# Performance work log

Hardware: AMD Instinct MI355X
Metric: run time of the kernel (lower is better)

The kernel has to match this reference:

```python
import jax, jax.numpy as jnp
import numpy as np
from jax import lax

B, L, R = 128, 256, 36
D_TXT, D_IMG, D_SOC = 768, 2048, 10
EPS = 0.05 ** 2        # geomloss blur=0.05, p=2 -> epsilon = blur^p
N_ITERS = 20           # fixed log-domain Sinkhorn iterations
GAMMA = 0.01


def _pcost(x, y):
    # x: [B,n,d], y: [B,m,d] -> C_ij = ||x_i - y_j||^2 / 2 (geomloss p=2 cost)
    xx = jnp.sum(x * x, -1)[:, :, None]
    yy = jnp.sum(y * y, -1)[:, None, :]
    xy = jnp.einsum('bnd,bmd->bnm', x, y)
    return 0.5 * (xx + yy - 2.0 * xy)


def _sinkhorn_cost(C, loga, logb, eps, n_iters):
    # Log-domain Sinkhorn; masked points carry loga/logb = -inf (zero weight).
    f = jnp.zeros(loga.shape, C.dtype)
    g = jnp.zeros(logb.shape, C.dtype)

    def body(fg, _):
        f, g = fg
        g = -eps * jax.nn.logsumexp(loga[:, :, None] + (f[:, :, None] - C) / eps, axis=1)
        f = -eps * jax.nn.logsumexp(logb[:, None, :] + (g[:, None, :] - C) / eps, axis=2)
        return (f, g), None

    (f, g), _ = lax.scan(body, (f, g), None, length=n_iters)
    a = jnp.exp(loga)  # exp(-inf) = 0 for masked entries
    b = jnp.exp(logb)
    return jnp.sum(a * f, -1) + jnp.sum(b * g, -1)  # <a,f> + <b,g>


def _forward(txt_global, txt_region, img_global, img_region, social, attn_mask,
             W_stat, b_stat, W_gt, b_gt, W_gi, b_gi, W_rt, b_rt, W_ri, b_ri,
             W_m1, b_m1, W_m2, b_m2):
    relu = jax.nn.relu
    soc = relu(social @ W_stat + b_stat)                            # [B,100]
    tg = relu(jnp.concatenate([txt_global, soc], axis=1) @ W_gt + b_gt)  # [B,200]
    ig = relu(img_global @ W_gi + b_gi)                              # [B,200]
    h = relu((tg + ig) @ W_m1 + b_m1)
    mix_pred = h @ W_m2 + b_m2                                       # [B,2]

    tr = relu(txt_region @ W_rt + b_rt)                              # [B,L,50]
    ir = relu(img_region @ W_ri + b_ri)                              # [B,R,50]

    Bn, _, _ = tr.shape
    Rn = ir.shape[1]
    mask = attn_mask > 0
    n_words = jnp.sum(attn_mask, axis=-1).astype(tr.dtype)          # [B]
    loga = jnp.where(mask, -jnp.log(n_words)[:, None], -jnp.inf)    # uniform over valid tokens
    logb = jnp.full((Bn, Rn), -jnp.log(float(Rn)), tr.dtype)        # uniform over regions

    # Debiased Sinkhorn divergence (geomloss SamplesLoss default debias=True):
    Sxy = _sinkhorn_cost(_pcost(tr, ir), loga, logb, EPS, N_ITERS)
    Sxx = _sinkhorn_cost(_pcost(tr, tr), loga, loga, EPS, N_ITERS)
    Syy = _sinkhorn_cost(_pcost(ir, ir), logb, logb, EPS, N_ITERS)
    w_dis = Sxy - 0.5 * (Sxx + Syy)                                  # [B]

    w_pred = jnp.stack([1.0 - GAMMA * w_dis, GAMMA * w_dis], axis=1)  # [B,2]
    logit = jax.nn.softmax(jnp.maximum(mix_pred, w_pred), axis=1)
    return logit


def setup_inputs() -> dict:
    key = jax.random.key(0)
    ks = jax.random.split(key, 24)
    init = lambda k, s: (jax.random.normal(k, s) * 0.02).astype(jnp.float32)
    lengths = jax.random.randint(ks[0], (B,), 16, L + 1)             # ragged lengths
    attn_mask = (jnp.arange(L)[None, :] < lengths[:, None]).astype(jnp.int32)
    return {
        'txt_global': jax.random.normal(ks[1], (B, D_TXT), jnp.float32),
        'txt_region': jax.random.normal(ks[2], (B, L, D_TXT), jnp.float32),
        'img_global': jax.random.normal(ks[3], (B, D_IMG), jnp.float32),
        'img_region': jax.random.normal(ks[4], (B, R, D_IMG), jnp.float32),
        'social': jax.random.normal(ks[5], (B, D_SOC), jnp.float32),
        'attn_mask': attn_mask,
        'W_stat': init(ks[6], (D_SOC, 100)), 'b_stat': jnp.zeros((100,), jnp.float32),
        'W_gt': init(ks[7], (868, 200)), 'b_gt': jnp.zeros((200,), jnp.float32),
        'W_gi': init(ks[8], (D_IMG, 200)), 'b_gi': jnp.zeros((200,), jnp.float32),
        'W_rt': init(ks[9], (D_TXT, 50)), 'b_rt': jnp.zeros((50,), jnp.float32),
        'W_ri': init(ks[10], (D_IMG, 50)), 'b_ri': jnp.zeros((50,), jnp.float32),
        'W_m1': init(ks[11], (200, 100)), 'b_m1': jnp.zeros((100,), jnp.float32),
        'W_m2': init(ks[12], (100, 2)), 'b_m2': jnp.zeros((2,), jnp.float32),
    }


def reference(txt_global, txt_region, img_global, img_region, social, attn_mask,
              W_stat, b_stat, W_gt, b_gt, W_gi, b_gi, W_rt, b_rt, W_ri, b_ri,
              W_m1, b_m1, W_m2, b_m2):
    return _forward(txt_global, txt_region, img_global, img_region, social, attn_mask,
                    W_stat, b_stat, W_gt, b_gt, W_gi, b_gi, W_rt, b_rt, W_ri, b_ri,
                    W_m1, b_m1, W_m2, b_m2)
```

## Files before the change

### kernel.cpp

```cpp
#include <hip/hip_runtime.h>

typedef float        f32x4 __attribute__((ext_vector_type(4)));
typedef short        s16x8 __attribute__((ext_vector_type(8)));
typedef unsigned int u32x4 __attribute__((ext_vector_type(4)));

#define EPS_LN2      0.0017328679513998632f
#define INV_EPS_LN2  577.0780163555852f
#define LOG2_36      5.169925001442312f

__device__ __forceinline__ short f2bf(float x) {
  unsigned int u; __builtin_memcpy(&u, &x, 4);
  u = (u + 0x7FFFu + ((u >> 16) & 1u)) >> 16;
  return (short)u;
}

__device__ __forceinline__ unsigned short f2h(float x) {
  return __builtin_bit_cast(unsigned short, (_Float16)x);
}
__device__ __forceinline__ float h2f(unsigned short h) {
  return (float)__builtin_bit_cast(_Float16, h);
}

#define GLOAD16(g, l) __builtin_amdgcn_global_load_lds( \
    (const __attribute__((address_space(1))) void*)(g), \
    (__attribute__((address_space(3))) void*)(l), 16, 0, 0)

__global__ __launch_bounds__(256) void k_prep(
    const float* __restrict__ W_rt, const float* __restrict__ W_ri,
    short* __restrict__ frt, short* __restrict__ fri,
    const float* __restrict__ txt, const float* __restrict__ img,
    const float* __restrict__ social,
    const float* __restrict__ W_stat, const float* __restrict__ b_stat,
    const float* __restrict__ W_gt, const float* __restrict__ W_gi,
    float* __restrict__ pre) {
  __shared__ float sA[32][128];
  int bid = blockIdx.x;
  if (bid < 88) {
    int slot = bid * 256 + threadIdx.x;
    const float* W; short* dst; int f;
    if (slot < 6144) { W = W_rt; dst = frt; f = slot; }
    else             { W = W_ri; dst = fri; f = slot - 6144; }
    int k32 = f >> 8, rem = f & 255, ct = rem >> 6, l = rem & 63;
    int col = ct * 16 + (l & 15);
    int k0  = k32 * 32 + (l >> 4) * 8;
    s16x8 p;
#pragma unroll
    for (int c = 0; c < 8; ++c) {
      float v = (col < 50) ? W[(k0 + c) * 50 + col] : 0.f;
      p[c] = f2bf(v);
    }
    *(s16x8*)(dst + (long)f * 8) = p;
    return;
  }
  int gb = bid - 88;
  int job = gb >> 4, rb = (gb >> 2) & 3, cb = gb & 3;
  int t = threadIdx.x, r0 = rb * 32;
  const float* W; int k0, klen;
  if (job < 6)       { k0 = job * 128;       klen = 128; W = W_gt; }
  else if (job == 6) { k0 = 0;               klen = 100; W = W_gt + 768 * 200; }
  else               { k0 = (job - 7) * 128; klen = 128; W = W_gi; }
  if (job == 6) {
    for (int idx = t; idx < 4096; idx += 256) {
      int r = idx >> 7, k = idx & 127;
      float v = 0.f;
      if (k < 100) {
        v = b_stat[k];
#pragma unroll
        for (int u = 0; u < 10; ++u) v += social[(r0 + r) * 10 + u] * W_stat[u * 100 + k];
        v = fmaxf(v, 0.f);
      }
      sA[r][k] = v;
    }
  } else {
    const float* A = (job < 6) ? txt : img;
    int K_A = (job < 6) ? 768 : 2048;
    for (int idx = t; idx < 4096; idx += 256) {
      int r = idx >> 7, k = idx & 127;
      sA[r][k] = A[(r0 + r) * K_A + k0 + k];
    }
  }
  __syncthreads();
  int c = cb * 64 + (t & 63), rg = t >> 6;
  if (c < 200) {
    float acc[8];
#pragma unroll
    for (int i = 0; i < 8; ++i) acc[i] = 0.f;
    for (int k4 = 0; k4 < klen; k4 += 4) {
      float w0 = W[(k0 + k4    ) * 200 + c];
      float w1 = W[(k0 + k4 + 1) * 200 + c];
      float w2 = W[(k0 + k4 + 2) * 200 + c];
      float w3 = W[(k0 + k4 + 3) * 200 + c];
#pragma unroll
      for (int i = 0; i < 8; ++i) {
        f32x4 a = *(const f32x4*)&sA[rg * 8 + i][k4];
        acc[i] += a[0]*w0 + a[1]*w1 + a[2]*w2 + a[3]*w3;
      }
    }
    float* dst = pre + (long)job * 25600;
#pragma unroll
    for (int i = 0; i < 8; ++i)
      dst[(r0 + rg * 8 + i) * 200 + c] = acc[i];
  }
}

template<int K32>
__device__ __forceinline__ void proj_body(const float* __restrict__ A,
                                          const short* __restrict__ Bf,
                                          const float* __restrict__ bias,
                                          float* __restrict__ out, int bid,
                                          char* smem) {
  constexpr int KH = K32 / 2;
  int wave = threadIdx.x >> 6, lane = threadIdx.x & 63;
  int rg = wave >> 1, ks = wave & 1;
  int rl = lane & 15, q = lane >> 4, r7 = rl & 7;
  int row0 = bid * 32 + rg * 16;
  const int K = K32 * 32;
  char* wbuf = smem + wave * 12288;

  int ra = lane >> 3, pa = lane & 7;
  int fsw = (pa ^ ra) * 4;
  const float* asrc0 = A + (long)(row0 + ra)     * K + ks * (KH * 32) + fsw;
  const float* asrc1 = A + (long)(row0 + 8 + ra) * K + ks * (KH * 32) + fsw;
  const short* bsrc  = Bf + (long)ks * (KH * 2048) + lane * 8;

#define PSTAGE(KK, ST) { \
    char* ad = wbuf + (ST) * 6144; \
    GLOAD16(asrc0 + (KK) * 32, ad); \
    GLOAD16(asrc1 + (KK) * 32, ad + 1024); \
    char* bd = ad + 2048; \
    const short* bs = bsrc + (KK) * 2048; \
    GLOAD16(bs,        bd); \
    GLOAD16(bs + 512,  bd + 1024); \
    GLOAD16(bs + 1024, bd + 2048); \
    GLOAD16(bs + 1536, bd + 3072); \
  }

  f32x4 acc[4];
#pragma unroll
  for (int ct = 0; ct < 4; ++ct) acc[ct] = (f32x4){0.f, 0.f, 0.f, 0.f};

  PSTAGE(0, 0);
#pragma unroll
  for (int k = 0; k < KH; ++k) {
    if (k + 1 < KH) {
      PSTAGE(k + 1, (k + 1) & 1);
      asm volatile("s_waitcnt vmcnt(6)" ::: "memory");
    } else {
      asm volatile("s_waitcnt vmcnt(0)" ::: "memory");
    }
    __builtin_amdgcn_sched_barrier(0);
    const char* ab = wbuf + (k & 1) * 6144;
    f32x4 a0 = *(const f32x4*)(ab + rl * 128 + (((q * 2)     ^ r7) << 4));
    f32x4 a1 = *(const f32x4*)(ab + rl * 128 + (((q * 2 + 1) ^ r7) << 4));
    const char* bb = ab + 2048;
    s16x8 af;
    af[0]=f2bf(a0[0]); af[1]=f2bf(a0[1]); af[2]=f2bf(a0[2]); af[3]=f2bf(a0[3]);
    af[4]=f2bf(a1[0]); af[5]=f2bf(a1[1]); af[6]=f2bf(a1[2]); af[7]=f2bf(a1[3]);
#pragma unroll
    for (int ct = 0; ct < 4; ++ct) {
      s16x8 bfr = *(const s16x8*)(bb + ct * 1024 + lane * 16);
      acc[ct] = __builtin_amdgcn_mfma_f32_16x16x32_bf16(af, bfr, acc[ct], 0, 0, 0);
    }
  }
#undef PSTAGE

  if (ks == 1) {
#pragma unroll
    for (int ct = 0; ct < 4; ++ct)
      *(f32x4*)(wbuf + ct * 1024 + lane * 16) = acc[ct];
  }
  __syncthreads();
  if (ks == 0) {
    const char* pb = smem + (wave + 1) * 12288;
#pragma unroll
    for (int ct = 0; ct < 4; ++ct) {
      f32x4 o = *(const f32x4*)(pb + ct * 1024 + lane * 16);
      int col = ct * 16 + rl;
      float bv = (col < 50) ? bias[col] : 0.f;
#pragma unroll
      for (int r = 0; r < 4; ++r) {
        int grow = row0 + q * 4 + r;
        float v = fmaxf(acc[ct][r] + o[r] + bv, 0.f);
        out[(long)grow * 64 + col] = (col < 50) ? v : 0.f;
      }
    }
  }
}

__device__ __forceinline__ void mix_body(
    int r, const float* __restrict__ pre,
    const float* __restrict__ b_gt, const float* __restrict__ b_gi,
    const float* __restrict__ W_m1, const float* __restrict__ b_m1,
    const float* __restrict__ W_m2, const float* __restrict__ b_m2,
    float* __restrict__ mix, float* smem) {
  float* sm = smem;
  float* sh = smem + 200;
  int t = threadIdx.x;
  if (t < 200) {
    float s1 = b_gt[t], s2 = b_gi[t];
#pragma unroll
    for (int j = 0; j < 7; ++j)  s1 += pre[(long)j * 25600 + r * 200 + t];
#pragma unroll
    for (int j = 7; j < 23; ++j) s2 += pre[(long)j * 25600 + r * 200 + t];
    sm[t] = fmaxf(s1, 0.f) + fmaxf(s2, 0.f);
  }
  __syncthreads();
  if (t < 100) {
    float a = b_m1[t];
#pragma unroll 4
    for (int k = 0; k < 200; ++k) a += sm[k] * W_m1[k * 100 + t];
    sh[t] = fmaxf(a, 0.f);
  }
  __syncthreads();
  if (t < 2) {
    float a = b_m2[t];
    for (int k = 0; k < 100; ++k) a += sh[k] * W_m2[k * 2 + t];
    mix[r * 2 + t] = a;
  }
}

__global__ __launch_bounds__(256)
void k_pm(
    const float* __restrict__ txt_region, const short* __restrict__ frt,
    const float* __restrict__ b_rt, float* __restrict__ tr,
    const float* __restrict__ img_region, const short* __restrict__ fri,
    const float* __restrict__ b_ri, float* __restrict__ ir,
    const float* __restrict__ pre,
    const float* __restrict__ b_gt, const float* __restrict__ b_gi,
    const float* __restrict__ W_m1, const float* __restrict__ b_m1,
    const float* __restrict__ W_m2, const float* __restrict__ b_m2,
    float* __restrict__ mix) {
  __shared__ __align__(16) char smem[49152];
  int bid = blockIdx.x;
  if (bid < 144)       proj_body<64>(img_region, fri, b_ri, ir, bid, smem);
  else if (bid < 1168) proj_body<24>(txt_region, frt, b_rt, tr, bid - 144, smem);
  else                 mix_body(bid - 1168, pre, b_gt, b_gi, W_m1, b_m1, W_m2, b_m2, mix, (float*)smem);
}

#define SK_SMEM 139264

__global__ __launch_bounds__(1024)
void k_sink(
    const float* __restrict__ tr, const float* __restrict__ ir,
    const int* __restrict__ amask,
    float* __restrict__ Sxy, float* __restrict__ Sxx, float* __restrict__ Syy) {
  __shared__ __align__(16) char smem[SK_SMEM];
  int role = blockIdx.x >> 7;
  int b    = blockIdx.x & 127;
  int tid  = threadIdx.x;

  if (role == 0) {
    short*     Xf    = (short*)smem;
    char*      CT    = smem;
    float*     norms = (float*)(smem + 131072);
    float*     sPm   = (float*)(smem + 132096);
    float*     sF    = (float*)(smem + 136192);
    float*     sG    = (float*)(smem + 137216);
    _Float16*  sAh   = (_Float16*)(smem + 138240);
    int*       nsh   = (int*)  (smem + 138784);
    if (tid < 64) {
      int c = 0;
      for (int i = tid; i < 256; i += 64) c += amask[b * 256 + i];
#pragma unroll
      for (int o = 1; o < 64; o <<= 1) c += __shfl_xor(c, o);
      if (tid == 0) *nsh = c;
    }
    const float* Xg = tr + (long)b * 256 * 64;
    for (int slot = tid; slot < 2048; slot += 1024) {
      int t = slot >> 7, k32 = (slot >> 6) & 1, l = slot & 63;
      int row = t * 16 + (l & 15), k0 = k32 * 32 + (l >> 4) * 8;
      const float* src = Xg + row * 64 + k0;
      f32x4 a0 = *(const f32x4*)src, a1 = *(const f32x4*)(src + 4);
      s16x8 p;
      p[0]=f2bf(a0[0]); p[1]=f2bf(a0[1]); p[2]=f2bf(a0[2]); p[3]=f2bf(a0[3]);
      p[4]=f2bf(a1[0]); p[5]=f2bf(a1[1]); p[6]=f2bf(a1[2]); p[7]=f2bf(a1[3]);
      *(s16x8*)(Xf + slot * 8) = p;
    }
    __syncthreads();
    int n = *nsh;
    int wv = tid >> 6, lane = tid & 63, q = lane >> 4;
    f32x4 acc[16];
#pragma unroll
    for (int ct = 0; ct < 16; ++ct) acc[ct] = (f32x4){0.f, 0.f, 0.f, 0.f};
    s16x8 afr0 = *(const s16x8*)(Xf + ((wv * 2 + 0) * 64 + lane) * 8);
    s16x8 afr1 = *(const s16x8*)(Xf + ((wv * 2 + 1) * 64 + lane) * 8);
#pragma unroll
    for (int ct = 0; ct < 16; ++ct) {
      s16x8 b0 = *(const s16x8*)(Xf + ((ct * 2 + 0) * 64 + lane) * 8);
      s16x8 b1 = *(const s16x8*)(Xf + ((ct * 2 + 1) * 64 + lane) * 8);
      acc[ct] = __builtin_amdgcn_mfma_f32_16x16x32_bf16(afr0, b0, acc[ct], 0, 0, 0);
      acc[ct] = __builtin_amdgcn_mfma_f32_16x16x32_bf16(afr1, b1, acc[ct], 0, 0, 0);
    }
#pragma unroll
    for (int r = 0; r < 4; ++r) {
      int m_ = q * 4 + r;
      if ((lane & 15) == m_) norms[wv * 16 + m_] = acc[wv][r];
    }
    __syncthreads();
    int i0w = wv * 16 + q * 4;
    float ni0 = norms[i0w], ni1 = norms[i0w + 1];
    float ni2 = norms[i0w + 2], ni3 = norms[i0w + 3];
#pragma unroll
    for (int ct = 0; ct < 16; ++ct) {
      int j = ct * 16 + (lane & 15);
      float nj = norms[j];
      float v0 = (acc[ct][0] - 0.5f * (ni0 + nj)) * INV_EPS_LN2;
      float v1 = (acc[ct][1] - 0.5f * (ni1 + nj)) * INV_EPS_LN2;
      float v2 = (acc[ct][2] - 0.5f * (ni2 + nj)) * INV_EPS_LN2;
      float v3 = (acc[ct][3] - 0.5f * (ni3 + nj)) * INV_EPS_LN2;
      char* p = CT + (((j << 9) + (i0w << 1)) ^ ((j & 7) << 4));
      unsigned p01 = (unsigned)f2h(v0) | ((unsigned)f2h(v1) << 16);
      unsigned p23 = (unsigned)f2h(v2) | ((unsigned)f2h(v3) << 16);
      *(unsigned*)(p)     = p01;
      *(unsigned*)(p + 4) = p23;
    }
    float log2n = log2f((float)n);
    if (tid < 256) {
      sF[tid] = 0.f;
      sAh[tid] = (tid < n) ? (_Float16)(-log2n) : (_Float16)(-65504.f);
    }
    __syncthreads();
    int kk = tid >> 8, j = tid & 255, i0 = kk * 64;
    unsigned base = (unsigned)((j << 9) + (i0 << 1));
    unsigned sw   = (unsigned)((j & 7) << 4);
    const unsigned* ah2 = (const unsigned*)(sAh) + kk * 32;
    for (int h = 0; h < 40; ++h) {
      unsigned mm = 0xFBFFFBFFu;
#pragma unroll
      for (int s = 0; s < 8; ++s) {
        u32x4 v = *(const u32x4*)(CT + ((base + (s << 4)) ^ sw));
        unsigned a0 = ah2[s * 4 + 0], a1 = ah2[s * 4 + 1];
        unsigned a2 = ah2[s * 4 + 2], a3 = ah2[s * 4 + 3];
        unsigned t0, t1, t2, t3;
        asm("v_pk_add_f16 %0, %1, %2" : "=v"(t0) : "v"(v[0]), "v"(a0));
        asm("v_pk_add_f16 %0, %1, %2" : "=v"(t1) : "v"(v[1]), "v"(a1));
        asm("v_pk_add_f16 %0, %1, %2" : "=v"(t2) : "v"(v[2]), "v"(a2));
        asm("v_pk_add_f16 %0, %1, %2" : "=v"(t3) : "v"(v[3]), "v"(a3));
        asm("v_pk_max_f16 %0, %0, %1" : "+v"(mm) : "v"(t0));
        asm("v_pk_max_f16 %0, %0, %1" : "+v"(mm) : "v"(t1));
        asm("v_pk_max_f16 %0, %0, %1" : "+v"(mm) : "v"(t2));
        asm("v_pk_max_f16 %0, %0, %1" : "+v"(mm) : "v"(t3));
      }
      sPm[kk * 256 + j] = fmaxf(h2f((unsigned short)(mm & 0xFFFFu)),
                                h2f((unsigned short)(mm >> 16)));
      __syncthreads();
      if (tid < 256) {
        float m4 = fmaxf(fmaxf(sPm[tid], sPm[256 + tid]),
                         fmaxf(sPm[512 + tid], sPm[768 + tid]));
        if (tid < n) {
          ((h & 1) ? sF : sG)[tid] = -EPS_LN2 * m4;
          sAh[tid] = (_Float16)(-log2n - m4);
        }
      }
      __syncthreads();
    }
    if (tid < 64) {
      float a = 0.f;
      for (int i = tid; i < n; i += 64) a += sF[i] + sG[i];
#pragma unroll
      for (int o = 1; o < 64; o <<= 1) a += __shfl_xor(a, o);
      if (tid == 0) Sxx[b] = a / n;
    }
  } else if (role == 1) {
    float* Ys  = (float*)smem;
    float* Cs  = (float*)(smem + 9216);
    float* nx  = (float*)(smem + 47104);
    float* ny  = (float*)(smem + 48128);
    float* sA  = (float*)(smem + 48288);
    float* sB  = (float*)(smem + 49376);
    float* sF  = (float*)(smem + 49536);
    float* sG  = (float*)(smem + 50560);
    int*   nsh = (int*)  (smem + 50720);
    if (tid < 64) {
      int c = 0;
      for (int i = tid; i < 256; i += 64) c += amask[b * 256 + i];
#pragma unroll
      for (int o = 1; o < 64; o <<= 1) c += __shfl_xor(c, o);
      if (tid == 0) *nsh = c;
    }
    const float* Xg = tr + (long)b * 256 * 64;
    const float* Yg = ir + (long)b * 36 * 64;
    for (int idx = tid; idx < 576; idx += 1024) {
      int row = idx >> 4, q4 = idx & 15;
      *(f32x4*)(Ys + row * 64 + q4 * 4) = *(const f32x4*)(Yg + row * 64 + q4 * 4);
    }
    __syncthreads();
    int n = *nsh;
    if (tid < 256) {
      float a = 0.f;
#pragma unroll
      for (int q4 = 0; q4 < 13; ++q4) {
        f32x4 v = *(const f32x4*)(Xg + tid * 64 + q4 * 4);
        a += v[0]*v[0] + v[1]*v[1] + v[2]*v[2] + v[3]*v[3];
      }
      nx[tid] = a;
    } else if (tid < 292) {
      int jj = tid - 256; float a = 0.f;
#pragma unroll
      for (int q4 = 0; q4 < 13; ++q4) {
        f32x4 v = *(const f32x4*)(Ys + jj * 64 + q4 * 4);
        a += v[0]*v[0] + v[1]*v[1] + v[2]*v[2] + v[3]*v[3];
      }
      ny[jj] = a;
    }
    __syncthreads();
    if (tid < 1008) {
      int ii = tid / 36, jj = tid - ii * 36;
      f32x4 yr[13];
#pragma unroll
      for (int q4 = 0; q4 < 13; ++q4) yr[q4] = *(const f32x4*)(Ys + jj * 64 + q4 * 4);
      float nyj = ny[jj];
      for (int i = ii; i < 256; i += 28) {
        float d = 0.f;
#pragma unroll
        for (int q4 = 0; q4 < 13; ++q4) {
          f32x4 xv = *(const f32x4*)(Xg + i * 64 + q4 * 4);
          d += xv[0]*yr[q4][0] + xv[1]*yr[q4][1] + xv[2]*yr[q4][2] + xv[3]*yr[q4][3];
        }
        Cs[i * 37 + jj] = (d - 0.5f * (nx[i] + nyj)) * INV_EPS_LN2;
      }
    }
    __syncthreads();
    int jg = tid >> 4, kg = tid & 15;
    float Cg[16];
    if (jg < 36) {
#pragma unroll
      for (int t = 0; t < 16; ++t) Cg[t] = Cs[(kg * 16 + t) * 37 + jg];
    }
    int fi = tid >> 2, kf = tid & 3;
    float Cf[9];
#pragma unroll
    for (int t = 0; t < 9; ++t) {
      int jj2 = kf * 9 + t;
      Cf[t] = (jj2 < 36) ? Cs[fi * 37 + jj2] : 0.f;
    }
    float log2n = log2f((float)n);
    if (tid < 256) { sF[tid] = 0.f; sA[tid + (tid >> 4)] = -log2n; }
    __syncthreads();
    const float* agp = sA + kg * 17;
    int gend = n - kg * 16; if (gend > 16) gend = 16;
    for (int it = 0; it < 20; ++it) {
      float gm = -1e30f;
      if (jg < 36) {
#pragma unroll
        for (int t = 0; t < 16; ++t)
          if (t < gend) gm = fmaxf(gm, agp[t] + Cg[t]);
        gm = fmaxf(gm, __shfl_xor(gm, 1)); gm = fmaxf(gm, __shfl_xor(gm, 2));
        gm = fmaxf(gm, __shfl_xor(gm, 4)); gm = fmaxf(gm, __shfl_xor(gm, 8));
      }
      __syncthreads();
      if (jg < 36 && kg == 0) {
        sG[jg] = -EPS_LN2 * gm;
        sB[jg] = -LOG2_36 - gm;
      }
      __syncthreads();
      float fm = -1e30f;
#pragma unroll
      for (int t = 0; t < 9; ++t) {
        int jj2 = kf * 9 + t;
        if (jj2 < 36) fm = fmaxf(fm, sB[jj2] + Cf[t]);
      }
      fm = fmaxf(fm, __shfl_xor(fm, 1)); fm = fmaxf(fm, __shfl_xor(fm, 2));
      __syncthreads();
      if (kf == 0 && fi < n) {
        sF[fi] = -EPS_LN2 * fm;
        sA[fi + (fi >> 4)] = -log2n - fm;
      }
      __syncthreads();
    }
    if (tid < 64) {
      float a = 0.f;
      for (int i = tid; i < n; i += 64) a += sF[i];
      float g = (tid < 36) ? sG[tid] : 0.f;
#pragma unroll
      for (int o = 1; o < 64; o <<= 1) { a += __shfl_xor(a, o); g += __shfl_xor(g, o); }
      if (tid == 0) Sxy[b] = a / n + g / 36.f;
    }
  } else {
    float* Ys = (float*)smem;
    float* Cs = (float*)(smem + 9216);
    float* ny = (float*)(smem + 48128);
    float* sA = (float*)(smem + 48288);
    float* sF = (float*)(smem + 49536);
    float* sG = (float*)(smem + 50560);
    const float* Yg = ir + (long)b * 36 * 64;
    for (int idx = tid; idx < 576; idx += 1024) {
      int row = idx >> 4, q4 = idx & 15;
      *(f32x4*)(Ys + row * 64 + q4 * 4) = *(const f32x4*)(Yg + row * 64 + q4 * 4);
    }
    __syncthreads();
    if (tid < 36) {
      float a = 0.f;
#pragma unroll
      for (int q4 = 0; q4 < 13; ++q4) {
        f32x4 v = *(const f32x4*)(Ys + tid * 64 + q4 * 4);
        a += v[0]*v[0] + v[1]*v[1] + v[2]*v[2] + v[3]*v[3];
      }
      ny[tid] = a;
    }
    __syncthreads();
    if (tid < 1008) {
      int ii = tid / 36, jj = tid - ii * 36;
      f32x4 yr[13];
#pragma unroll
      for (int q4 = 0; q4 < 13; ++q4) yr[q4] = *(const f32x4*)(Ys + jj * 64 + q4 * 4);
      float nyj = ny[jj];
      for (int i = ii; i < 36; i += 28) {
        float d = 0.f;
#pragma unroll
        for (int q4 = 0; q4 < 13; ++q4) {
          f32x4 xv = *(const f32x4*)(Ys + i * 64 + q4 * 4);
          d += xv[0]*yr[q4][0] + xv[1]*yr[q4][1] + xv[2]*yr[q4][2] + xv[3]*yr[q4][3];
        }
        Cs[i * 37 + jj] = (d - 0.5f * (ny[i] + nyj)) * INV_EPS_LN2;
      }
    }
    __syncthreads();
    int j = tid >> 2, kk = tid & 3;
    float Creg[9];
    if (j < 36) {
#pragma unroll
      for (int t = 0; t < 9; ++t) {
        int i2 = kk * 9 + t;
        Creg[t] = (i2 < 36) ? Cs[i2 * 37 + j] : 0.f;
      }
    }
    if (tid < 36) { sF[tid] = 0.f; sA[tid] = -LOG2_36; }
    __syncthreads();
    for (int h = 0; h < 40; ++h) {
      float m = -1e30f;
      if (j < 36) {
#pragma unroll
        for (int t = 0; t < 9; ++t) {
          int i2 = kk * 9 + t;
          if (i2 < 36) m = fmaxf(m, sA[i2] + Creg[t]);
        }
        m = fmaxf(m, __shfl_xor(m, 1)); m = fmaxf(m, __shfl_xor(m, 2));
      }
      __syncthreads();
      if (j < 36 && kk == 0) {
        ((h & 1) ? sF : sG)[j] = -EPS_LN2 * m;
        sA[j] = -LOG2_36 - m;
      }
      __syncthreads();
    }
    if (tid < 64) {
      float a = (tid < 36) ? sF[tid] + sG[tid] : 0.f;
#pragma unroll
      for (int o = 1; o < 64; o <<= 1) a += __shfl_xor(a, o);
      if (tid == 0) Syy[b] = a / 36.f;
    }
  }
}

__global__ void k_final(const float* __restrict__ mix, const float* __restrict__ sxy,
                        const float* __restrict__ sxx, const float* __restrict__ syy,
                        float* __restrict__ out) {
  int b = blockIdx.x * 64 + threadIdx.x;
  if (b < 128) {
    float w  = sxy[b] - 0.5f * (sxx[b] + syy[b]);
    float x0 = fmaxf(mix[b * 2 + 0], 1.0f - 0.01f * w);
    float x1 = fmaxf(mix[b * 2 + 1], 0.01f * w);
    float mx = fmaxf(x0, x1);
    float e0 = expf(x0 - mx), e1 = expf(x1 - mx);
    float inv = 1.f / (e0 + e1);
    out[b * 2 + 0] = e0 * inv;
    out[b * 2 + 1] = e1 * inv;
  }
}

extern "C" void kernel_launch(void* const* d_in, const int* in_sizes, int n_in,
                              void* d_out, int out_size, void* d_ws, size_t ws_size,
                              hipStream_t stream) {
  const float* txt_global = (const float*)d_in[0];
  const float* txt_region = (const float*)d_in[1];
  const float* img_global = (const float*)d_in[2];
  const float* img_region = (const float*)d_in[3];
  const float* social     = (const float*)d_in[4];
  const int*   attn_mask  = (const int*)  d_in[5];
  const float* W_stat = (const float*)d_in[6];  const float* b_stat = (const float*)d_in[7];
  const float* W_gt   = (const float*)d_in[8];  const float* b_gt   = (const float*)d_in[9];
  const float* W_gi   = (const float*)d_in[10]; const float* b_gi   = (const float*)d_in[11];
  const float* W_rt   = (const float*)d_in[12]; const float* b_rt   = (const float*)d_in[13];
  const float* W_ri   = (const float*)d_in[14]; const float* b_ri   = (const float*)d_in[15];
  const float* W_m1   = (const float*)d_in[16]; const float* b_m1   = (const float*)d_in[17];
  const float* W_m2   = (const float*)d_in[18]; const float* b_m2   = (const float*)d_in[19];

  float* ws = (float*)d_ws;
  float* ws_mix = ws;
  float* ws_sxy = ws + 256;
  float* ws_sxx = ws + 384;
  float* ws_syy = ws + 512;
  short* ws_frt = (short*)(ws + 1024);
  short* ws_fri = (short*)(ws + 25600);
  float* ws_tr  = ws + 131072;
  float* ws_ir  = ws + 2228224;
  float* ws_pre = ws + 2523136;

  k_prep<<<456, 256, 0, stream>>>(W_rt, W_ri, ws_frt, ws_fri,
                                  txt_global, img_global, social,
                                  W_stat, b_stat, W_gt, W_gi, ws_pre);
  k_pm<<<1296, 256, 0, stream>>>(txt_region, ws_frt, b_rt, ws_tr,
                                 img_region, ws_fri, b_ri, ws_ir,
                                 ws_pre, b_gt, b_gi,
                                 W_m1, b_m1, W_m2, b_m2, ws_mix);
  k_sink<<<384, 1024, 0, stream>>>(ws_tr, ws_ir, attn_mask,
                                   ws_sxy, ws_sxx, ws_syy);
  k_final<<<2, 64, 0, stream>>>(ws_mix, ws_sxy, ws_sxx, ws_syy, (float*)d_out);
}
```

Baseline: 326.4 us.

## Split Sxx Sinkhorn into separate 256-thread kernel and triple-buffer projection loads

Moves the text-text self Sinkhorn out of the fused 1024-thread kernel into its own 256-thread kernel. Each thread owns one column and scans only the valid rows, with ping-pong f16 potential buffers, so the per-iteration partial-max exchange and one barrier go away. The projection GEMM changes from double to triple buffering of its global-to-LDS loads, with deeper vmcnt waits. The costs are fewer threads per Sxx block, an extra kernel launch, a larger LDS footprint in k_pm that may lower occupancy, and a round trip through global memory for the row norms.

New measurement: 399.6 us. +22.4%, slower.

```diff
diff --git a/kernel.cpp b/kernel.cpp
--- a/kernel.cpp
+++ b/kernel.cpp
@@ -115,7 +115,7 @@
   int rl = lane & 15, q = lane >> 4, r7 = rl & 7;
   int row0 = bid * 32 + rg * 16;
   const int K = K32 * 32;
-  char* wbuf = smem + wave * 12288;
+  char* wbuf = smem + wave * 18432;
 
   int ra = lane >> 3, pa = lane & 7;
   int fsw = (pa ^ ra) * 4;
@@ -140,16 +140,19 @@
   for (int ct = 0; ct < 4; ++ct) acc[ct] = (f32x4){0.f, 0.f, 0.f, 0.f};
 
   PSTAGE(0, 0);
+  PSTAGE(1, 1);
 #pragma unroll
   for (int k = 0; k < KH; ++k) {
-    if (k + 1 < KH) {
-      PSTAGE(k + 1, (k + 1) & 1);
+    if (k + 2 < KH) {
+      PSTAGE(k + 2, (k + 2) % 3);
+      asm volatile("s_waitcnt vmcnt(12)" ::: "memory");
+    } else if (k + 2 == KH) {
       asm volatile("s_waitcnt vmcnt(6)" ::: "memory");
     } else {
       asm volatile("s_waitcnt vmcnt(0)" ::: "memory");
     }
     __builtin_amdgcn_sched_barrier(0);
-    const char* ab = wbuf + (k & 1) * 6144;
+    const char* ab = wbuf + (k % 3) * 6144;
     f32x4 a0 = *(const f32x4*)(ab + rl * 128 + (((q * 2)     ^ r7) << 4));
     f32x4 a1 = *(const f32x4*)(ab + rl * 128 + (((q * 2 + 1) ^ r7) << 4));
     const char* bb = ab + 2048;
@@ -171,7 +174,7 @@
   }
   __syncthreads();
   if (ks == 0) {
-    const char* pb = smem + (wave + 1) * 12288;
+    const char* pb = smem + (wave + 1) * 18432;
 #pragma unroll
     for (int ct = 0; ct < 4; ++ct) {
       f32x4 o = *(const f32x4*)(pb + ct * 1024 + lane * 16);
@@ -230,105 +233,115 @@
     const float* __restrict__ W_m1, const float* __restrict__ b_m1,
     const float* __restrict__ W_m2, const float* __restrict__ b_m2,
     float* __restrict__ mix) {
-  __shared__ __align__(16) char smem[49152];
+  __shared__ __align__(16) char smem[73728];
   int bid = blockIdx.x;
   if (bid < 144)       proj_body<64>(img_region, fri, b_ri, ir, bid, smem);
   else if (bid < 1168) proj_body<24>(txt_region, frt, b_rt, tr, bid - 144, smem);
   else                 mix_body(bid - 1168, pre, b_gt, b_gi, W_m1, b_m1, W_m2, b_m2, mix, (float*)smem);
 }
 
-#define SK_SMEM 139264
-
-__global__ __launch_bounds__(1024)
-void k_sink(
-    const float* __restrict__ tr, const float* __restrict__ ir,
-    const int* __restrict__ amask,
-    float* __restrict__ Sxy, float* __restrict__ Sxx, float* __restrict__ Syy) {
-  __shared__ __align__(16) char smem[SK_SMEM];
-  int role = blockIdx.x >> 7;
-  int b    = blockIdx.x & 127;
-  int tid  = threadIdx.x;
-
-  if (role == 0) {
-    short*     Xf    = (short*)smem;
-    char*      CT    = smem;
-    float*     norms = (float*)(smem + 131072);
-    float*     sPm   = (float*)(smem + 132096);
-    float*     sF    = (float*)(smem + 136192);
-    float*     sG    = (float*)(smem + 137216);
-    _Float16*  sAh   = (_Float16*)(smem + 138240);
-    int*       nsh   = (int*)  (smem + 138784);
-    if (tid < 64) {
-      int c = 0;
-      for (int i = tid; i < 256; i += 64) c += amask[b * 256 + i];
-#pragma unroll
-      for (int o = 1; o < 64; o <<= 1) c += __shfl_xor(c, o);
-      if (tid == 0) *nsh = c;
-    }
-    const float* Xg = tr + (long)b * 256 * 64;
-    for (int slot = tid; slot < 2048; slot += 1024) {
-      int t = slot >> 7, k32 = (slot >> 6) & 1, l = slot & 63;
-      int row = t * 16 + (l & 15), k0 = k32 * 32 + (l >> 4) * 8;
-      const float* src = Xg + row * 64 + k0;
-      f32x4 a0 = *(const f32x4*)src, a1 = *(const f32x4*)(src + 4);
-      s16x8 p;
-      p[0]=f2bf(a0[0]); p[1]=f2bf(a0[1]); p[2]=f2bf(a0[2]); p[3]=f2bf(a0[3]);
-      p[4]=f2bf(a1[0]); p[5]=f2bf(a1[1]); p[6]=f2bf(a1[2]); p[7]=f2bf(a1[3]);
-      *(s16x8*)(Xf + slot * 8) = p;
-    }
-    __syncthreads();
-    int n = *nsh;
-    int wv = tid >> 6, lane = tid & 63, q = lane >> 4;
+__global__ __launch_bounds__(256) void k_sxx(
+    const float* __restrict__ tr, const int* __restrict__ amask,
+    float* __restrict__ norms_g, float* __restrict__ Sxx) {
+  __shared__ __align__(16) char smem[163840];
+  char*  CT = smem;
+  short* Xf = (short*)(smem + 131072);
+  float*     sF   = (float*)(smem + 131072);
+  float*     sG   = (float*)(smem + 132096);
+  _Float16*  sA0  = (_Float16*)(smem + 133120);
+  _Float16*  sA1  = (_Float16*)(smem + 133632);
+  int b = blockIdx.x, tid = threadIdx.x;
+  int lane = tid & 63, wv = tid >> 6;
+  int q = lane >> 4, rl = lane & 15;
+
+  int c = 0;
+#pragma unroll
+  for (int i = 0; i < 4; ++i) c += amask[b * 256 + i * 64 + lane];
+#pragma unroll
+  for (int o = 1; o < 64; o <<= 1) c += __shfl_xor(c, o);
+  int n = __builtin_amdgcn_readfirstlane(c);
+
+  const float* Xg = tr + (long)b * 256 * 64;
+  for (int slot = tid; slot < 2048; slot += 256) {
+    int t = slot >> 7, k32 = (slot >> 6) & 1, l = slot & 63;
+    int row = t * 16 + (l & 15), k0 = k32 * 32 + (l >> 4) * 8;
+    const float* src = Xg + row * 64 + k0;
+    f32x4 a0 = *(const f32x4*)src, a1 = *(const f32x4*)(src + 4);
+    s16x8 p;
+    p[0]=f2bf(a0[0]); p[1]=f2bf(a0[1]); p[2]=f2bf(a0[2]); p[3]=f2bf(a0[3]);
+    p[4]=f2bf(a1[0]); p[5]=f2bf(a1[1]); p[6]=f2bf(a1[2]); p[7]=f2bf(a1[3]);
+    *(s16x8*)(Xf + slot * 8) = p;
+  }
+  __syncthreads();
+
+  float* ng = norms_g + b * 256;
+#pragma unroll
+  for (int si = 0; si < 4; ++si) {
+    int st = wv * 4 + si;
+    s16x8 a0 = *(const s16x8*)(Xf + ((st * 2 + 0) * 64 + lane) * 8);
+    s16x8 a1 = *(const s16x8*)(Xf + ((st * 2 + 1) * 64 + lane) * 8);
+    f32x4 d = (f32x4){0.f, 0.f, 0.f, 0.f};
+    d = __builtin_amdgcn_mfma_f32_16x16x32_bf16(a0, a0, d, 0, 0, 0);
+    d = __builtin_amdgcn_mfma_f32_16x16x32_bf16(a1, a1, d, 0, 0, 0);
+#pragma unroll
+    for (int r = 0; r < 4; ++r)
+      if (rl == q * 4 + r) ng[st * 16 + q * 4 + r] = d[r];
+  }
+  __syncthreads();
+
+  float nj[16];
+#pragma unroll
+  for (int ct = 0; ct < 16; ++ct) nj[ct] = ng[ct * 16 + rl];
+
+#pragma unroll
+  for (int si = 0; si < 4; ++si) {
+    int st = wv * 4 + si;
+    int i0w = st * 16 + q * 4;
+    float ni0 = ng[i0w], ni1 = ng[i0w + 1], ni2 = ng[i0w + 2], ni3 = ng[i0w + 3];
+    s16x8 a0 = *(const s16x8*)(Xf + ((st * 2 + 0) * 64 + lane) * 8);
+    s16x8 a1 = *(const s16x8*)(Xf + ((st * 2 + 1) * 64 + lane) * 8);
     f32x4 acc[16];
 #pragma unroll
     for (int ct = 0; ct < 16; ++ct) acc[ct] = (f32x4){0.f, 0.f, 0.f, 0.f};
-    s16x8 afr0 = *(const s16x8*)(Xf + ((wv * 2 + 0) * 64 + lane) * 8);
-    s16x8 afr1 = *(const s16x8*)(Xf + ((wv * 2 + 1) * 64 + lane) * 8);
 #pragma unroll
     for (int ct = 0; ct < 16; ++ct) {
       s16x8 b0 = *(const s16x8*)(Xf + ((ct * 2 + 0) * 64 + lane) * 8);
       s16x8 b1 = *(const s16x8*)(Xf + ((ct * 2 + 1) * 64 + lane) * 8);
-      acc[ct] = __builtin_amdgcn_mfma_f32_16x16x32_bf16(afr0, b0, acc[ct], 0, 0, 0);
-      acc[ct] = __builtin_amdgcn_mfma_f32_16x16x32_bf16(afr1, b1, acc[ct], 0, 0, 0);
-    }
-#pragma unroll
-    for (int r = 0; r < 4; ++r) {
-      int m_ = q * 4 + r;
-      if ((lane & 15) == m_) norms[wv * 16 + m_] = acc[wv][r];
-    }
-    __syncthreads();
-    int i0w = wv * 16 + q * 4;
-    float ni0 = norms[i0w], ni1 = norms[i0w + 1];
-    float ni2 = norms[i0w + 2], ni3 = norms[i0w + 3];
+      acc[ct] = __builtin_amdgcn_mfma_f32_16x16x32_bf16(a0, b0, acc[ct], 0, 0, 0);
+      acc[ct] = __builtin_amdgcn_mfma_f32_16x16x32_bf16(a1, b1, acc[ct], 0, 0, 0);
+    }
 #pragma unroll
     for (int ct = 0; ct < 16; ++ct) {
-      int j = ct * 16 + (lane & 15);
-      float nj = norms[j];
-      float v0 = (acc[ct][0] - 0.5f * (ni0 + nj)) * INV_EPS_LN2;
-      float v1 = (acc[ct][1] - 0.5f * (ni1 + nj)) * INV_EPS_LN2;
-      float v2 = (acc[ct][2] - 0.5f * (ni2 + nj)) * INV_EPS_LN2;
-      float v3 = (acc[ct][3] - 0.5f * (ni3 + nj)) * INV_EPS_LN2;
+      int j = ct * 16 + rl;
+      float njv = nj[ct];
+      float v0 = (acc[ct][0] - 0.5f * (ni0 + njv)) * INV_EPS_LN2;
+      float v1 = (acc[ct][1] - 0.5f * (ni1 + njv)) * INV_EPS_LN2;
+      float v2 = (acc[ct][2] - 0.5f * (ni2 + njv)) * INV_EPS_LN2;
+      float v3 = (acc[ct][3] - 0.5f * (ni3 + njv)) * INV_EPS_LN2;
       char* p = CT + (((j << 9) + (i0w << 1)) ^ ((j & 7) << 4));
-      unsigned p01 = (unsigned)f2h(v0) | ((unsigned)f2h(v1) << 16);
-      unsigned p23 = (unsigned)f2h(v2) | ((unsigned)f2h(v3) << 16);
-      *(unsigned*)(p)     = p01;
-      *(unsigned*)(p + 4) = p23;
-    }
-    float log2n = log2f((float)n);
-    if (tid < 256) {
-      sF[tid] = 0.f;
-      sAh[tid] = (tid < n) ? (_Float16)(-log2n) : (_Float16)(-65504.f);
-    }
-    __syncthreads();
-    int kk = tid >> 8, j = tid & 255, i0 = kk * 64;
-    unsigned base = (unsigned)((j << 9) + (i0 << 1));
-    unsigned sw   = (unsigned)((j & 7) << 4);
-    const unsigned* ah2 = (const unsigned*)(sAh) + kk * 32;
-    for (int h = 0; h < 40; ++h) {
+      *(unsigned*)(p)     = (unsigned)f2h(v0) | ((unsigned)f2h(v1) << 16);
+      *(unsigned*)(p + 4) = (unsigned)f2h(v2) | ((unsigned)f2h(v3) << 16);
+    }
+  }
+  __syncthreads();
+
+  float log2n = log2f((float)n);
+  sF[tid] = 0.f; sG[tid] = 0.f;
+  sA0[tid] = (tid < n) ? (_Float16)(-log2n) : (_Float16)(-65504.f);
+  sA1[tid] = (_Float16)(-65504.f);
+  __syncthreads();
+
+  int j = tid;
+  unsigned base = (unsigned)(j << 9);
+  unsigned sw   = (unsigned)((j & 7) << 4);
+  int ns = (n + 7) >> 3;
+  for (int h = 0; h < 40; ++h) {
+    const unsigned* ah2 = (const unsigned*)((h & 1) ? sA1 : sA0);
+    _Float16* aout = (h & 1) ? sA0 : sA1;
+    if (j < n) {
       unsigned mm = 0xFBFFFBFFu;
-#pragma unroll
-      for (int s = 0; s < 8; ++s) {
-        u32x4 v = *(const u32x4*)(CT + ((base + (s << 4)) ^ sw));
+      for (int s = 0; s < ns; ++s) {
+        u32x4 v = *(const u32x4*)(CT + ((base + (unsigned)(s << 4)) ^ sw));
         unsigned a0 = ah2[s * 4 + 0], a1 = ah2[s * 4 + 1];
         unsigned a2 = ah2[s * 4 + 2], a3 = ah2[s * 4 + 3];
         unsigned t0, t1, t2, t3;
@@ -341,27 +354,34 @@
         asm("v_pk_max_f16 %0, %0, %1" : "+v"(mm) : "v"(t2));
         asm("v_pk_max_f16 %0, %0, %1" : "+v"(mm) : "v"(t3));
       }
-      sPm[kk * 256 + j] = fmaxf(h2f((unsigned short)(mm & 0xFFFFu)),
-                                h2f((unsigned short)(mm >> 16)));
-      __syncthreads();
-      if (tid < 256) {
-        float m4 = fmaxf(fmaxf(sPm[tid], sPm[256 + tid]),
-                         fmaxf(sPm[512 + tid], sPm[768 + tid]));
-        if (tid < n) {
-          ((h & 1) ? sF : sG)[tid] = -EPS_LN2 * m4;
-          sAh[tid] = (_Float16)(-log2n - m4);
-        }
-      }
-      __syncthreads();
-    }
-    if (tid < 64) {
-      float a = 0.f;
-      for (int i = tid; i < n; i += 64) a += sF[i] + sG[i];
-#pragma unroll
-      for (int o = 1; o < 64; o <<= 1) a += __shfl_xor(a, o);
-      if (tid == 0) Sxx[b] = a / n;
-    }
-  } else if (role == 1) {
+      float m = fmaxf(h2f((unsigned short)(mm & 0xFFFFu)),
+                      h2f((unsigned short)(mm >> 16)));
+      ((h & 1) ? sF : sG)[j] = -EPS_LN2 * m;
+      aout[j] = (_Float16)(-log2n - m);
+    }
+    __syncthreads();
+  }
+  if (tid < 64) {
+    float a = 0.f;
+    for (int i = tid; i < n; i += 64) a += sF[i] + sG[i];
+#pragma unroll
+    for (int o = 1; o < 64; o <<= 1) a += __shfl_xor(a, o);
+    if (tid == 0) Sxx[b] = a / n;
+  }
+}
+
+#define SK_SMEM 50736
+
+__global__ __launch_bounds__(1024) void k_sxy(
+    const float* __restrict__ tr, const float* __restrict__ ir,
+    const int* __restrict__ amask,
+    float* __restrict__ Sxy, float* __restrict__ Syy) {
+  __shared__ __align__(16) char smem[SK_SMEM];
+  int role = blockIdx.x >> 7;
+  int b    = blockIdx.x & 127;
+  int tid  = threadIdx.x;
+
+  if (role == 0) {
     float* Ys  = (float*)smem;
     float* Cs  = (float*)(smem + 9216);
     float* nx  = (float*)(smem + 47104);
@@ -596,6 +616,7 @@
   float* ws_tr  = ws + 131072;
   float* ws_ir  = ws + 2228224;
   float* ws_pre = ws + 2523136;
+  float* ws_nrm = ws + 3111936;
 
   k_prep<<<456, 256, 0, stream>>>(W_rt, W_ri, ws_frt, ws_fri,
                                   txt_global, img_global, social,
@@ -604,7 +625,7 @@
                                  img_region, ws_fri, b_ri, ws_ir,
                                  ws_pre, b_gt, b_gi,
                                  W_m1, b_m1, W_m2, b_m2, ws_mix);
-  k_sink<<<384, 1024, 0, stream>>>(ws_tr, ws_ir, attn_mask,
-                                   ws_sxy, ws_sxx, ws_syy);
+  k_sxx<<<128, 256, 0, stream>>>(ws_tr, attn_mask, ws_nrm, ws_sxx);
+  k_sxy<<<256, 1024, 0, stream>>>(ws_tr, ws_ir, attn_mask, ws_sxy, ws_syy);
   k_final<<<2, 64, 0, stream>>>(ws_mix, ws_sxy, ws_sxx, ws_syy, (float*)d_out);
 }
```
